# Kernel optimization log

Hardware: AMD Instinct MI355X
Metric: run time of the kernel (lower is better)

The kernel has to match this reference:

```python
import jax, jax.numpy as jnp
import numpy as np

NEG_INF = -9e15  # matches -9000000000000000.0 in torch code
ALPHA = 0.2      # LeakyReLU negative slope


def setup_inputs() -> dict:
    key = jax.random.key(0)
    k1, k2, k3, k4 = jax.random.split(key, 4)
    B, N, Fin, Fout = 8, 2048, 256, 256
    h = jax.random.normal(k1, (B, N, Fin), dtype=jnp.float32)
    adj = jax.random.randint(k2, (B, N, N), 0, 2, dtype=jnp.int32)
    W = jax.random.normal(k3, (Fin, Fout), dtype=jnp.float32) * 0.05
    a = jax.random.normal(k4, (2 * Fout, 1), dtype=jnp.float32) * 0.05
    return {"h": h, "adj": adj, "W": W, "a": a}


def reference(h, adj, W, a):
    # h: [B,N,Fin], adj: [B,N,N], W: [Fin,Fout], a: [2*Fout,1]
    Fout = W.shape[1]
    Wh = jnp.matmul(h, W)                       # [B,N,Fout]
    # Decompose concat-based additive score: e_ij = LReLU(a1.Wh_i + a2.Wh_j)
    a1 = a[:Fout, 0]                            # source-node part
    a2 = a[Fout:, 0]                            # target-node part
    s1 = jnp.einsum('bnf,f->bn', Wh, a1)        # [B,N]
    s2 = jnp.einsum('bnf,f->bn', Wh, a2)        # [B,N]
    e = jax.nn.leaky_relu(s1[:, :, None] + s2[:, None, :], negative_slope=ALPHA)  # [B,N,N]
    attn = jnp.where(adj > 0, e, NEG_INF)
    attn = jax.nn.softmax(attn, axis=2)          # masked softmax over neighbors
    # dropout omitted (deterministic eval-mode reference)
    h_prime = jnp.matmul(attn, Wh)               # [B,N,Fout]
    return h_prime
```

## Files before the change

kernel.cpp:

```cpp
#include <hip/hip_runtime.h>
#include <cstdint>

#define ALPHA 0.2f

constexpr int NB = 8;
constexpr int NN = 2048;
constexpr int NF = 256;

typedef __attribute__((ext_vector_type(8))) short bf16x8;
typedef __attribute__((ext_vector_type(4))) float f32x4;

__device__ __forceinline__ float bf2f(unsigned short u) {
    union { unsigned int i; float f; } v;
    v.i = ((unsigned int)u) << 16;
    return v.f;
}
__device__ __forceinline__ unsigned short f2bf(float f) {
    union { float f; unsigned int i; } v;
    v.f = f;
    v.i += 0x7fffu + ((v.i >> 16) & 1);
    return (unsigned short)(v.i >> 16);
}

__global__ __launch_bounds__(256) void k_wt(const float* __restrict__ W,
                                            unsigned short* __restrict__ WT,
                                            float* __restrict__ s1,
                                            float* __restrict__ s2) {
    const int t = threadIdx.x;
    const int gid = blockIdx.x * 256 + t;
    s1[gid] = 0.f;
    s2[gid] = 0.f;
    const int k = blockIdx.x * 4 + (t >> 6);
    const int f0 = (t & 63) * 4;
    const float4 w = *(const float4*)&W[k * NF + f0];
    WT[(f0 + 0) * NF + k] = f2bf(w.x);
    WT[(f0 + 1) * NF + k] = f2bf(w.y);
    WT[(f0 + 2) * NF + k] = f2bf(w.z);
    WT[(f0 + 3) * NF + k] = f2bf(w.w);
}

__global__ __launch_bounds__(256, 4) void k_wh(const float* __restrict__ h,
                                               const unsigned short* __restrict__ WT,
                                               const float* __restrict__ a,
                                               unsigned short* __restrict__ WhT,
                                               float* __restrict__ s1,
                                               float* __restrict__ s2) {
    __shared__ __align__(16) unsigned short As[64][72];
    __shared__ __align__(16) unsigned short Bs[64][72];
    const int tid = threadIdx.x;
    const int lane = tid & 63;
    const int l16 = lane & 15;
    const int quad = lane >> 4;
    const int wave = tid >> 6;

    const int p = blockIdx.x;
    const int xcd = p & 7;
    const int q = p >> 3;
    const int rowTile = xcd + (q >> 2) * 8;
    const int row0 = rowTile * 64;
    const int col0 = (q & 3) * 64;

    const int bb = row0 >> 11;
    const int n0 = row0 & (NN - 1);
    const int mb = (wave & 1) * 32;
    const int nb = (wave >> 1) * 32;

    f32x4 acc[2][2];
#pragma unroll
    for (int mf = 0; mf < 2; ++mf)
#pragma unroll
        for (int nf = 0; nf < 2; ++nf) acc[mf][nf] = (f32x4){0.f, 0.f, 0.f, 0.f};

    const int r0 = tid >> 4;
    const int k4 = (tid & 15) * 4;
    const int f0w = tid >> 3;
    const int k8 = (tid & 7) * 8;

    const float* hP = &h[(size_t)(row0 + r0) * NF + k4];
    const unsigned short* wP = &WT[(size_t)(col0 + f0w) * NF + k8];

    float4 h0, h1, h2, h3;
    uint4 wv0, wv1;

#define LOADW(K0)                                                      \
    do {                                                               \
        h0 = *(const float4*)&hP[(size_t)(0 * 16) * NF + (K0)];        \
        h1 = *(const float4*)&hP[(size_t)(1 * 16) * NF + (K0)];        \
        h2 = *(const float4*)&hP[(size_t)(2 * 16) * NF + (K0)];        \
        h3 = *(const float4*)&hP[(size_t)(3 * 16) * NF + (K0)];        \
        wv0 = *(const uint4*)&wP[(K0)];                                \
        wv1 = *(const uint4*)&wP[(size_t)32 * NF + (K0)];              \
    } while (0)

    LOADW(0);

    for (int k0 = 0; k0 < NF; k0 += 64) {
        ushort4 o;
        o.x = f2bf(h0.x); o.y = f2bf(h0.y); o.z = f2bf(h0.z); o.w = f2bf(h0.w);
        *(ushort4*)&As[r0 + 0][k4] = o;
        o.x = f2bf(h1.x); o.y = f2bf(h1.y); o.z = f2bf(h1.z); o.w = f2bf(h1.w);
        *(ushort4*)&As[r0 + 16][k4] = o;
        o.x = f2bf(h2.x); o.y = f2bf(h2.y); o.z = f2bf(h2.z); o.w = f2bf(h2.w);
        *(ushort4*)&As[r0 + 32][k4] = o;
        o.x = f2bf(h3.x); o.y = f2bf(h3.y); o.z = f2bf(h3.z); o.w = f2bf(h3.w);
        *(ushort4*)&As[r0 + 48][k4] = o;
        *(uint4*)&Bs[f0w][k8] = wv0;
        *(uint4*)&Bs[f0w + 32][k8] = wv1;
        __syncthreads();
        if (k0 + 64 < NF) LOADW(k0 + 64);
#pragma unroll
        for (int ks = 0; ks < 64; ks += 32) {
            bf16x8 av[2], bv[2];
#pragma unroll
            for (int mf = 0; mf < 2; ++mf)
                av[mf] = *(const bf16x8*)&As[mb + mf * 16 + l16][ks + quad * 8];
#pragma unroll
            for (int nf = 0; nf < 2; ++nf)
                bv[nf] = *(const bf16x8*)&Bs[nb + nf * 16 + l16][ks + quad * 8];
#pragma unroll
            for (int mf = 0; mf < 2; ++mf)
#pragma unroll
                for (int nf = 0; nf < 2; ++nf)
                    acc[mf][nf] = __builtin_amdgcn_mfma_f32_16x16x32_bf16(
                        av[mf], bv[nf], acc[mf][nf], 0, 0, 0);
        }
        __syncthreads();
    }
#undef LOADW

#pragma unroll
    for (int mf = 0; mf < 2; ++mf) {
#pragma unroll
        for (int nf = 0; nf < 2; ++nf) {
            const size_t f = col0 + nb + nf * 16 + l16;
            const int nr = n0 + mb + mf * 16 + quad * 4;
            ushort4 o;
            o.x = f2bf(acc[mf][nf][0]);
            o.y = f2bf(acc[mf][nf][1]);
            o.z = f2bf(acc[mf][nf][2]);
            o.w = f2bf(acc[mf][nf][3]);
            *(ushort4*)&WhT[((size_t)bb * NF + f) * NN + nr] = o;
        }
    }

    float a1v[2], a2v[2];
#pragma unroll
    for (int nf = 0; nf < 2; ++nf) {
        const int f = col0 + nb + nf * 16 + l16;
        a1v[nf] = a[f];
        a2v[nf] = a[NF + f];
    }
#pragma unroll
    for (int mf = 0; mf < 2; ++mf) {
#pragma unroll
        for (int r = 0; r < 4; ++r) {
            float p1 = acc[mf][0][r] * a1v[0] + acc[mf][1][r] * a1v[1];
            float p2 = acc[mf][0][r] * a2v[0] + acc[mf][1][r] * a2v[1];
            p1 += __shfl_xor(p1, 1); p2 += __shfl_xor(p2, 1);
            p1 += __shfl_xor(p1, 2); p2 += __shfl_xor(p2, 2);
            p1 += __shfl_xor(p1, 4); p2 += __shfl_xor(p2, 4);
            p1 += __shfl_xor(p1, 8); p2 += __shfl_xor(p2, 8);
            if (l16 == 0) {
                const int n = n0 + mb + mf * 16 + quad * 4 + r;
                atomicAdd(&s1[bb * NN + n], p1);
                atomicAdd(&s2[bb * NN + n], p2);
            }
        }
    }
}

__global__ __launch_bounds__(256, 4) void k_attn(const unsigned short* __restrict__ WhT,
                                                 const int* __restrict__ adj,
                                                 const float* __restrict__ s1g,
                                                 const float* __restrict__ s2g,
                                                 float* __restrict__ out) {
    __shared__ __align__(16) unsigned short Pb[32][72];
    __shared__ float s1_s[32];
    __shared__ float l_s[32];

    const int tid = threadIdx.x;
    const int lane = tid & 63;
    const int l16 = lane & 15;
    const int quad = lane >> 4;
    const int wave = tid >> 6;
    const int bb = blockIdx.x & 7;
    const int rest = blockIdx.x >> 3;
    const int i0 = (rest >> 1) * 32;
    const int fbase = (rest & 1) * 128 + wave * 32;

    if (tid < 32) {
        s1_s[tid] = s1g[bb * NN + i0 + tid];
        l_s[tid] = 0.f;
    }
    __syncthreads();

    f32x4 acc[2][2];
#pragma unroll
    for (int m = 0; m < 2; ++m)
#pragma unroll
        for (int nf = 0; nf < 2; ++nf) acc[m][nf] = (f32x4){0.f, 0.f, 0.f, 0.f};

    const size_t whtBase = (size_t)bb * NF * NN;
    const size_t adjBase = (size_t)bb * NN * NN;

    const int pIr = tid >> 4;
    const int pKq = (tid & 15) * 4;
    const int* adjP0 = &adj[adjBase + (size_t)(i0 + pIr) * NN + pKq];
    const int* adjP1 = adjP0 + 16 * NN;
    const float* s2P = &s2g[bb * NN + pKq];

    const unsigned short* whB0 = &WhT[whtBase + (size_t)(fbase + l16) * NN + quad * 8];
    const unsigned short* whB1 = whB0 + (size_t)16 * NN;

    int4 am0, am1;
    float4 sv0;
    am0 = *(const int4*)&adjP0[0];
    am1 = *(const int4*)&adjP1[0];
    sv0 = *(const float4*)&s2P[0];

    for (int t = 0; t < NN / 64; ++t) {
        const int j0 = t * 64;
#pragma unroll
        for (int it = 0; it < 2; ++it) {
            const int ir = pIr + it * 16;
            const int4 av = it ? am1 : am0;
            const float s1v = s1_s[ir];
            float x0 = s1v + sv0.x, x1 = s1v + sv0.y;
            float x2 = s1v + sv0.z, x3 = s1v + sv0.w;
            x0 = x0 > 0.f ? x0 : ALPHA * x0;
            x1 = x1 > 0.f ? x1 : ALPHA * x1;
            x2 = x2 > 0.f ? x2 : ALPHA * x2;
            x3 = x3 > 0.f ? x3 : ALPHA * x3;
            const float p0 = av.x > 0 ? __expf(x0) : 0.f;
            const float p1 = av.y > 0 ? __expf(x1) : 0.f;
            const float p2 = av.z > 0 ? __expf(x2) : 0.f;
            const float p3 = av.w > 0 ? __expf(x3) : 0.f;
            uint2 pk;
            pk.x = (unsigned int)f2bf(p0) | ((unsigned int)f2bf(p1) << 16);
            pk.y = (unsigned int)f2bf(p2) | ((unsigned int)f2bf(p3) << 16);
            *(uint2*)&Pb[ir][pKq] = pk;
            float ps = (p0 + p1) + (p2 + p3);
            ps += __shfl_xor(ps, 8);
            ps += __shfl_xor(ps, 4);
            ps += __shfl_xor(ps, 2);
            ps += __shfl_xor(ps, 1);
            if ((tid & 15) == 0) l_s[ir] += ps;
        }
        const uint4 b00 = *(const uint4*)&whB0[j0];
        const uint4 b01 = *(const uint4*)&whB0[j0 + 32];
        const uint4 b10 = *(const uint4*)&whB1[j0];
        const uint4 b11 = *(const uint4*)&whB1[j0 + 32];
        __syncthreads();
        if (t + 1 < NN / 64) {
            am0 = *(const int4*)&adjP0[j0 + 64];
            am1 = *(const int4*)&adjP1[j0 + 64];
            sv0 = *(const float4*)&s2P[j0 + 64];
        }
        {
            bf16x8 a0 = *(const bf16x8*)&Pb[l16][quad * 8];
            bf16x8 a1 = *(const bf16x8*)&Pb[16 + l16][quad * 8];
            acc[0][0] = __builtin_amdgcn_mfma_f32_16x16x32_bf16(
                a0, *(const bf16x8*)&b00, acc[0][0], 0, 0, 0);
            acc[1][0] = __builtin_amdgcn_mfma_f32_16x16x32_bf16(
                a1, *(const bf16x8*)&b00, acc[1][0], 0, 0, 0);
            acc[0][1] = __builtin_amdgcn_mfma_f32_16x16x32_bf16(
                a0, *(const bf16x8*)&b10, acc[0][1], 0, 0, 0);
            acc[1][1] = __builtin_amdgcn_mfma_f32_16x16x32_bf16(
                a1, *(const bf16x8*)&b10, acc[1][1], 0, 0, 0);
            a0 = *(const bf16x8*)&Pb[l16][32 + quad * 8];
            a1 = *(const bf16x8*)&Pb[16 + l16][32 + quad * 8];
            acc[0][0] = __builtin_amdgcn_mfma_f32_16x16x32_bf16(
                a0, *(const bf16x8*)&b01, acc[0][0], 0, 0, 0);
            acc[1][0] = __builtin_amdgcn_mfma_f32_16x16x32_bf16(
                a1, *(const bf16x8*)&b01, acc[1][0], 0, 0, 0);
            acc[0][1] = __builtin_amdgcn_mfma_f32_16x16x32_bf16(
                a0, *(const bf16x8*)&b11, acc[0][1], 0, 0, 0);
            acc[1][1] = __builtin_amdgcn_mfma_f32_16x16x32_bf16(
                a1, *(const bf16x8*)&b11, acc[1][1], 0, 0, 0);
        }
        __syncthreads();
    }

    if (tid < 32) l_s[tid] = 1.0f / l_s[tid];
    __syncthreads();

#pragma unroll
    for (int m = 0; m < 2; ++m) {
#pragma unroll
        for (int r = 0; r < 4; ++r) {
            const int row = m * 16 + quad * 4 + r;
            const float inv = l_s[row];
#pragma unroll
            for (int nf = 0; nf < 2; ++nf) {
                out[((size_t)bb * NN + i0 + row) * NF + fbase + nf * 16 + l16] =
                    acc[m][nf][r] * inv;
            }
        }
    }
}

extern "C" void kernel_launch(void* const* d_in, const int* in_sizes, int n_in,
                              void* d_out, int out_size, void* d_ws, size_t ws_size,
                              hipStream_t stream) {
    const float* h = (const float*)d_in[0];
    const int* adj = (const int*)d_in[1];
    const float* W = (const float*)d_in[2];
    const float* a = (const float*)d_in[3];
    float* out = (float*)d_out;

    unsigned short* WhT = (unsigned short*)d_ws;
    float* s1 = (float*)((char*)d_ws + (size_t)NB * NN * NF * sizeof(unsigned short));
    float* s2 = s1 + (size_t)NB * NN;
    unsigned short* WT = (unsigned short*)(s2 + (size_t)NB * NN);

    k_wt<<<dim3(64), dim3(256), 0, stream>>>(W, WT, s1, s2);
    k_wh<<<dim3((NB * NN / 64) * (NF / 64)), dim3(256), 0, stream>>>(h, WT, a, WhT, s1, s2);
    k_attn<<<dim3(NB * (NN / 32) * 2), dim3(256), 0, stream>>>(WhT, adj, s1, s2, out);
}
```

Before: 263.9 us.

## Compute softmax probabilities in registers per wave, removing LDS staging and barriers

Each wave now computes its own exp-scores directly in the MFMA A-operand register layout instead of sharing them through an LDS tile guarded by two block barriers per step. This removes the LDS round trip and __syncthreads, and the row sums are reduced with shuffles. The cost is redundant work: the four waves in a block each recompute the same 32x64 probability tile and each reloads the adjacency mask, so exp work and adj traffic per block rise fourfold. Higher register use (launch bounds drop to 3 blocks per CU) and cheaper bf16 packing via perm are also included.

```diff
diff --git a/kernel.cpp b/kernel.cpp
--- a/kernel.cpp
+++ b/kernel.cpp
@@ -169,15 +169,25 @@
     }
 }
 
-__global__ __launch_bounds__(256, 4) void k_attn(const unsigned short* __restrict__ WhT,
+__device__ __forceinline__ unsigned int pk2bf(float lo, float hi) {
+    union { float f; unsigned int u; } a, b;
+    a.f = lo; b.f = hi;
+    return __builtin_amdgcn_perm(b.u + 0x8000u, a.u + 0x8000u, 0x07060302u);
+}
+__device__ __forceinline__ float pval(float s1v, float s2j, int a) {
+    float x = s1v + s2j;
+    x = fmaxf(x, ALPHA * x);
+    float e = __expf(x);
+    return a > 0 ? e : 0.f;
+}
+
+union U8 { bf16x8 v; unsigned int u[4]; };
+
+__global__ __launch_bounds__(256, 3) void k_attn(const unsigned short* __restrict__ WhT,
                                                  const int* __restrict__ adj,
                                                  const float* __restrict__ s1g,
                                                  const float* __restrict__ s2g,
                                                  float* __restrict__ out) {
-    __shared__ __align__(16) unsigned short Pb[32][72];
-    __shared__ float s1_s[32];
-    __shared__ float l_s[32];
-
     const int tid = threadIdx.x;
     const int lane = tid & 63;
     const int l16 = lane & 15;
@@ -188,108 +198,132 @@
     const int i0 = (rest >> 1) * 32;
     const int fbase = (rest & 1) * 128 + wave * 32;
 
-    if (tid < 32) {
-        s1_s[tid] = s1g[bb * NN + i0 + tid];
-        l_s[tid] = 0.f;
-    }
-    __syncthreads();
-
-    f32x4 acc[2][2];
-#pragma unroll
-    for (int m = 0; m < 2; ++m)
-#pragma unroll
-        for (int nf = 0; nf < 2; ++nf) acc[m][nf] = (f32x4){0.f, 0.f, 0.f, 0.f};
+    const int r0 = i0 + l16;
+    const int r1 = r0 + 16;
+    const float s1v0 = s1g[bb * NN + r0];
+    const float s1v1 = s1g[bb * NN + r1];
+
+    const size_t adjBase = (size_t)bb * NN * NN;
+    const int* adjR0 = &adj[adjBase + (size_t)r0 * NN + quad * 8];
+    const int* adjR1 = &adj[adjBase + (size_t)r1 * NN + quad * 8];
+    const float* s2P = &s2g[bb * NN + quad * 8];
 
     const size_t whtBase = (size_t)bb * NF * NN;
-    const size_t adjBase = (size_t)bb * NN * NN;
-
-    const int pIr = tid >> 4;
-    const int pKq = (tid & 15) * 4;
-    const int* adjP0 = &adj[adjBase + (size_t)(i0 + pIr) * NN + pKq];
-    const int* adjP1 = adjP0 + 16 * NN;
-    const float* s2P = &s2g[bb * NN + pKq];
-
     const unsigned short* whB0 = &WhT[whtBase + (size_t)(fbase + l16) * NN + quad * 8];
     const unsigned short* whB1 = whB0 + (size_t)16 * NN;
 
-    int4 am0, am1;
-    float4 sv0;
-    am0 = *(const int4*)&adjP0[0];
-    am1 = *(const int4*)&adjP1[0];
-    sv0 = *(const float4*)&s2P[0];
-
-    for (int t = 0; t < NN / 64; ++t) {
-        const int j0 = t * 64;
-#pragma unroll
-        for (int it = 0; it < 2; ++it) {
-            const int ir = pIr + it * 16;
-            const int4 av = it ? am1 : am0;
-            const float s1v = s1_s[ir];
-            float x0 = s1v + sv0.x, x1 = s1v + sv0.y;
-            float x2 = s1v + sv0.z, x3 = s1v + sv0.w;
-            x0 = x0 > 0.f ? x0 : ALPHA * x0;
-            x1 = x1 > 0.f ? x1 : ALPHA * x1;
-            x2 = x2 > 0.f ? x2 : ALPHA * x2;
-            x3 = x3 > 0.f ? x3 : ALPHA * x3;
-            const float p0 = av.x > 0 ? __expf(x0) : 0.f;
-            const float p1 = av.y > 0 ? __expf(x1) : 0.f;
-            const float p2 = av.z > 0 ? __expf(x2) : 0.f;
-            const float p3 = av.w > 0 ? __expf(x3) : 0.f;
-            uint2 pk;
-            pk.x = (unsigned int)f2bf(p0) | ((unsigned int)f2bf(p1) << 16);
-            pk.y = (unsigned int)f2bf(p2) | ((unsigned int)f2bf(p3) << 16);
-            *(uint2*)&Pb[ir][pKq] = pk;
-            float ps = (p0 + p1) + (p2 + p3);
-            ps += __shfl_xor(ps, 8);
-            ps += __shfl_xor(ps, 4);
-            ps += __shfl_xor(ps, 2);
-            ps += __shfl_xor(ps, 1);
-            if ((tid & 15) == 0) l_s[ir] += ps;
-        }
-        const uint4 b00 = *(const uint4*)&whB0[j0];
-        const uint4 b01 = *(const uint4*)&whB0[j0 + 32];
-        const uint4 b10 = *(const uint4*)&whB1[j0];
-        const uint4 b11 = *(const uint4*)&whB1[j0 + 32];
-        __syncthreads();
-        if (t + 1 < NN / 64) {
-            am0 = *(const int4*)&adjP0[j0 + 64];
-            am1 = *(const int4*)&adjP1[j0 + 64];
-            sv0 = *(const float4*)&s2P[j0 + 64];
-        }
-        {
-            bf16x8 a0 = *(const bf16x8*)&Pb[l16][quad * 8];
-            bf16x8 a1 = *(const bf16x8*)&Pb[16 + l16][quad * 8];
-            acc[0][0] = __builtin_amdgcn_mfma_f32_16x16x32_bf16(
-                a0, *(const bf16x8*)&b00, acc[0][0], 0, 0, 0);
-            acc[1][0] = __builtin_amdgcn_mfma_f32_16x16x32_bf16(
-                a1, *(const bf16x8*)&b00, acc[1][0], 0, 0, 0);
-            acc[0][1] = __builtin_amdgcn_mfma_f32_16x16x32_bf16(
-                a0, *(const bf16x8*)&b10, acc[0][1], 0, 0, 0);
-            acc[1][1] = __builtin_amdgcn_mfma_f32_16x16x32_bf16(
-                a1, *(const bf16x8*)&b10, acc[1][1], 0, 0, 0);
-            a0 = *(const bf16x8*)&Pb[l16][32 + quad * 8];
-            a1 = *(const bf16x8*)&Pb[16 + l16][32 + quad * 8];
-            acc[0][0] = __builtin_amdgcn_mfma_f32_16x16x32_bf16(
-                a0, *(const bf16x8*)&b01, acc[0][0], 0, 0, 0);
-            acc[1][0] = __builtin_amdgcn_mfma_f32_16x16x32_bf16(
-                a1, *(const bf16x8*)&b01, acc[1][0], 0, 0, 0);
-            acc[0][1] = __builtin_amdgcn_mfma_f32_16x16x32_bf16(
-                a0, *(const bf16x8*)&b11, acc[0][1], 0, 0, 0);
-            acc[1][1] = __builtin_amdgcn_mfma_f32_16x16x32_bf16(
-                a1, *(const bf16x8*)&b11, acc[1][1], 0, 0, 0);
-        }
-        __syncthreads();
-    }
-
-    if (tid < 32) l_s[tid] = 1.0f / l_s[tid];
-    __syncthreads();
+    f32x4 acc[2][2];
+#pragma unroll
+    for (int m = 0; m < 2; ++m)
+#pragma unroll
+        for (int nf = 0; nf < 2; ++nf) acc[m][nf] = (f32x4){0.f, 0.f, 0.f, 0.f};
+    float lsum0 = 0.f, lsum1 = 0.f;
+
+#define LOAD_ADJ(A0, A1, A2, A3, B0, B1, B2, B3, J)                           \
+    do {                                                                      \
+        A0 = *(const int4*)&adjR0[(J)];                                       \
+        A1 = *(const int4*)&adjR0[(J) + 4];                                   \
+        A2 = *(const int4*)&adjR0[(J) + 32];                                  \
+        A3 = *(const int4*)&adjR0[(J) + 36];                                  \
+        B0 = *(const int4*)&adjR1[(J)];                                       \
+        B1 = *(const int4*)&adjR1[(J) + 4];                                   \
+        B2 = *(const int4*)&adjR1[(J) + 32];                                  \
+        B3 = *(const int4*)&adjR1[(J) + 36];                                  \
+    } while (0)
+
+#define PROW(S1V, QA0, QA1, QA2, QA3, AV0, AV1, LSUM)                         \
+    {                                                                         \
+        const float p0 = pval(S1V, s2A.x, QA0.x);                             \
+        const float p1 = pval(S1V, s2A.y, QA0.y);                             \
+        const float p2 = pval(S1V, s2A.z, QA0.z);                             \
+        const float p3 = pval(S1V, s2A.w, QA0.w);                             \
+        const float p4 = pval(S1V, s2B.x, QA1.x);                             \
+        const float p5 = pval(S1V, s2B.y, QA1.y);                             \
+        const float p6 = pval(S1V, s2B.z, QA1.z);                             \
+        const float p7 = pval(S1V, s2B.w, QA1.w);                             \
+        const float q0 = pval(S1V, s2C.x, QA2.x);                             \
+        const float q1 = pval(S1V, s2C.y, QA2.y);                             \
+        const float q2 = pval(S1V, s2C.z, QA2.z);                             \
+        const float q3 = pval(S1V, s2C.w, QA2.w);                             \
+        const float q4 = pval(S1V, s2D.x, QA3.x);                             \
+        const float q5 = pval(S1V, s2D.y, QA3.y);                             \
+        const float q6 = pval(S1V, s2D.z, QA3.z);                             \
+        const float q7 = pval(S1V, s2D.w, QA3.w);                             \
+        LSUM += (((p0 + p1) + (p2 + p3)) + ((p4 + p5) + (p6 + p7))) +         \
+                (((q0 + q1) + (q2 + q3)) + ((q4 + q5) + (q6 + q7)));          \
+        U8 u0_, u1_;                                                          \
+        u0_.u[0] = pk2bf(p0, p1); u0_.u[1] = pk2bf(p2, p3);                   \
+        u0_.u[2] = pk2bf(p4, p5); u0_.u[3] = pk2bf(p6, p7);                   \
+        u1_.u[0] = pk2bf(q0, q1); u1_.u[1] = pk2bf(q2, q3);                   \
+        u1_.u[2] = pk2bf(q4, q5); u1_.u[3] = pk2bf(q6, q7);                   \
+        AV0 = u0_.v; AV1 = u1_.v;                                             \
+    }
+
+#define ITER(T, CA0, CA1, CA2, CA3, CB0, CB1, CB2, CB3,                       \
+             XA0, XA1, XA2, XA3, XB0, XB1, XB2, XB3)                          \
+    {                                                                         \
+        const int j0 = (T) * 64;                                              \
+        const float4 s2A = *(const float4*)&s2P[j0];                          \
+        const float4 s2B = *(const float4*)&s2P[j0 + 4];                      \
+        const float4 s2C = *(const float4*)&s2P[j0 + 32];                     \
+        const float4 s2D = *(const float4*)&s2P[j0 + 36];                     \
+        const uint4 b00 = *(const uint4*)&whB0[j0];                           \
+        const uint4 b01 = *(const uint4*)&whB0[j0 + 32];                      \
+        const uint4 b10 = *(const uint4*)&whB1[j0];                           \
+        const uint4 b11 = *(const uint4*)&whB1[j0 + 32];                      \
+        if ((T) + 1 < NN / 64)                                                \
+            LOAD_ADJ(XA0, XA1, XA2, XA3, XB0, XB1, XB2, XB3, j0 + 64);        \
+        bf16x8 av00, av01, av10, av11;                                        \
+        PROW(s1v0, CA0, CA1, CA2, CA3, av00, av01, lsum0)                     \
+        PROW(s1v1, CB0, CB1, CB2, CB3, av10, av11, lsum1)                     \
+        acc[0][0] = __builtin_amdgcn_mfma_f32_16x16x32_bf16(                  \
+            av00, *(const bf16x8*)&b00, acc[0][0], 0, 0, 0);                  \
+        acc[1][0] = __builtin_amdgcn_mfma_f32_16x16x32_bf16(                  \
+            av10, *(const bf16x8*)&b00, acc[1][0], 0, 0, 0);                  \
+        acc[0][1] = __builtin_amdgcn_mfma_f32_16x16x32_bf16(                  \
+            av00, *(const bf16x8*)&b10, acc[0][1], 0, 0, 0);                  \
+        acc[1][1] = __builtin_amdgcn_mfma_f32_16x16x32_bf16(                  \
+            av10, *(const bf16x8*)&b10, acc[1][1], 0, 0, 0);                  \
+        acc[0][0] = __builtin_amdgcn_mfma_f32_16x16x32_bf16(                  \
+            av01, *(const bf16x8*)&b01, acc[0][0], 0, 0, 0);                  \
+        acc[1][0] = __builtin_amdgcn_mfma_f32_16x16x32_bf16(                  \
+            av11, *(const bf16x8*)&b01, acc[1][0], 0, 0, 0);                  \
+        acc[0][1] = __builtin_amdgcn_mfma_f32_16x16x32_bf16(                  \
+            av01, *(const bf16x8*)&b11, acc[0][1], 0, 0, 0);                  \
+        acc[1][1] = __builtin_amdgcn_mfma_f32_16x16x32_bf16(                  \
+            av11, *(const bf16x8*)&b11, acc[1][1], 0, 0, 0);                  \
+    }
+
+    int4 cA0, cA1, cA2, cA3, cB0, cB1, cB2, cB3;
+    int4 nA0 = {0, 0, 0, 0}, nA1 = {0, 0, 0, 0}, nA2 = {0, 0, 0, 0},
+         nA3 = {0, 0, 0, 0}, nB0 = {0, 0, 0, 0}, nB1 = {0, 0, 0, 0},
+         nB2 = {0, 0, 0, 0}, nB3 = {0, 0, 0, 0};
+    LOAD_ADJ(cA0, cA1, cA2, cA3, cB0, cB1, cB2, cB3, 0);
+
+    for (int tt = 0; tt < NN / 128; ++tt) {
+        ITER(2 * tt, cA0, cA1, cA2, cA3, cB0, cB1, cB2, cB3,
+             nA0, nA1, nA2, nA3, nB0, nB1, nB2, nB3)
+        ITER(2 * tt + 1, nA0, nA1, nA2, nA3, nB0, nB1, nB2, nB3,
+             cA0, cA1, cA2, cA3, cB0, cB1, cB2, cB3)
+    }
+#undef ITER
+#undef PROW
+#undef LOAD_ADJ
+
+    float sum0 = lsum0;
+    sum0 += __shfl_xor(sum0, 16);
+    sum0 += __shfl_xor(sum0, 32);
+    float sum1 = lsum1;
+    sum1 += __shfl_xor(sum1, 16);
+    sum1 += __shfl_xor(sum1, 32);
 
 #pragma unroll
     for (int m = 0; m < 2; ++m) {
 #pragma unroll
         for (int r = 0; r < 4; ++r) {
             const int row = m * 16 + quad * 4 + r;
-            const float inv = l_s[row];
+            const float sv = m ? __shfl(sum1, quad * 4 + r) : __shfl(sum0, quad * 4 + r);
+            const float inv = 1.f / sv;
 #pragma unroll
             for (int nf = 0; nf < 2; ++nf) {
                 out[((size_t)bb * NN + i0 + row) * NF + fbase + nf * 16 + l16] =
```

Result: slower. 372.0 us (+40.9%).
